# Performance work log

Hardware: AMD Instinct MI355X
Metric: run time of the kernel (lower is better)

## Reference

```python
import jax, jax.numpy as jnp
import numpy as np
import math

D_MODEL = 1024
HEADS = 16
DK = D_MODEL // HEADS
SEQ = 4096
BATCH = 4
SCALE_BASE = 512.0
ROPE_BASE = 10000.0
GN_EPS = 1e-5


def _xpos(x):
    # x: [B, S, D]; RetNet-style xpos rotary with per-dim magnitude scale
    B, S, D = x.shape
    half = D // 2
    sv = (jnp.arange(0, D, 2, dtype=jnp.float32) + 0.4 * D) / (1.4 * D)      # [half]
    pos = jnp.arange(S, dtype=jnp.float32)
    scale = sv[None, :] ** (pos[:, None] / SCALE_BASE)                        # [S, half]
    inv_freq = 1.0 / (ROPE_BASE ** (jnp.arange(half, dtype=jnp.float32) / half))
    ang = pos[:, None] * inv_freq[None, :]                                    # [S, half]
    sin = jnp.repeat(jnp.sin(ang) * scale, 2, axis=-1)                        # [S, D] (duplicate_interleave)
    cos = jnp.repeat(jnp.cos(ang) * scale, 2, axis=-1)
    x1, x2 = x[..., ::2], x[..., 1::2]
    rot = jnp.stack((-x2, x1), axis=-1).reshape(x.shape)                      # rotate_every_two
    return x * cos[None] + rot * sin[None]


def _decay_D():
    # D[h, n, m] = gamma_h**(n-m) * (n >= m); n over d_k rows, m over seq cols
    gammas = 1.0 - jnp.exp(jnp.linspace(math.log(1.0 / 32), math.log(1.0 / 512), HEADS))
    n = jnp.arange(DK)[:, None]
    m = jnp.arange(SEQ)[None, :]
    mask = n >= m
    diff = jnp.maximum(n - m, 0).astype(jnp.float32)                          # avoid inf for n<m
    return jnp.where(mask[None], gammas[:, None, None] ** diff[None], 0.0)    # [H, DK, SEQ]


def _group_norm(y, gn_w, gn_b):
    # torch GroupNorm(HEADS, DK) applied to rows of length DK
    B, S, D = y.shape
    g = DK // HEADS
    z = y.reshape(-1, HEADS, g)
    mu = z.mean(axis=-1, keepdims=True)
    var = z.var(axis=-1, keepdims=True)
    z = (z - mu) * jax.lax.rsqrt(var + GN_EPS)
    z = z * gn_w.reshape(HEADS, g) + gn_b.reshape(HEADS, g)
    return z.reshape(B, S, D)


def setup_inputs():
    key = jax.random.key(0)
    ks = jax.random.split(key, 9)
    s_d = 1.0 / math.sqrt(D_MODEL)
    s_s = 1.0 / math.sqrt(SEQ)
    return {
        "q": jax.random.normal(ks[0], (BATCH, SEQ, D_MODEL), jnp.float32),
        "k": jax.random.normal(ks[1], (BATCH, SEQ, D_MODEL), jnp.float32),
        "v": jax.random.normal(ks[2], (BATCH, SEQ, D_MODEL), jnp.float32),
        "wq": jax.random.normal(ks[3], (D_MODEL, D_MODEL), jnp.float32) * s_d,
        "wk": jax.random.normal(ks[4], (D_MODEL, D_MODEL), jnp.float32) * s_d,
        "wv": jax.random.normal(ks[5], (D_MODEL, D_MODEL), jnp.float32) * s_d,
        "wo": jax.random.normal(ks[6], (D_MODEL, D_MODEL), jnp.float32) * s_d,
        "wg": jax.random.normal(ks[7], (D_MODEL, D_MODEL), jnp.float32) * s_d,
        "wx_w": jax.random.normal(ks[8], (DK, SEQ), jnp.float32) * s_s,
        "wx_b": jnp.zeros((DK,), jnp.float32),
        "gn_w": jnp.ones((DK,), jnp.float32),
        "gn_b": jnp.zeros((DK,), jnp.float32),
    }


def reference(q, k, v, wq, wk, wv, wo, wg, wx_w, wx_b, gn_w, gn_b):
    B, S, D = q.shape
    query = _xpos(q @ wq.T)
    keyx = _xpos(k @ wk.T)
    value = v @ wv.T
    qh = query.reshape(B, S, HEADS, DK).transpose(0, 2, 1, 3)   # [B,H,S,DK]
    kh = keyx.reshape(B, S, HEADS, DK).transpose(0, 2, 1, 3)
    vh = value.reshape(B, S, HEADS, DK).transpose(0, 2, 1, 3)
    # Linformer-style learnable projection over sequence: [B,H,DK,S] -> [B,H,DK,DK]
    kp = jnp.einsum('bhsd,es->bhde', kh, wx_w) + wx_b
    vp = jnp.einsum('bhsd,es->bhde', vh, wx_w) + wx_b
    Dt = _decay_D().transpose(0, 2, 1)                           # [H, S, DK]
    scores = jnp.einsum('bhsd,bhde->bhse', qh, kp) * Dt[None]    # [B,H,S,DK]
    attn = jax.nn.softmax(scores, axis=-1)
    y = jnp.einsum('bhse,bhfe->bhsf', attn, vp)                  # attn @ Vp^T -> [B,H,S,DK]
    y = y.transpose(0, 2, 1, 3).reshape(B, S, D)
    y = _group_norm(y, gn_w, gn_b)
    gate = (q @ wg.T) * y
    return (gate * jax.nn.sigmoid(gate)) @ wo.T
```

## Files before the change

kernel.cpp:

```cpp
#include <hip/hip_runtime.h>
#include <hip/hip_bf16.h>

#define DEVI __device__ __forceinline__

typedef __attribute__((ext_vector_type(8))) short  short8;
typedef __attribute__((ext_vector_type(4))) float  floatx4;
typedef __attribute__((ext_vector_type(8))) __bf16 bf16x8;

DEVI float b2f(unsigned short u){ union{unsigned int i; float f;} x; x.i=((unsigned int)u)<<16; return x.f; }
DEVI unsigned short f2b(float f){
  union{float ff; unsigned int i;} x; x.ff=f;
  unsigned int r = x.i + 0x7fffu + ((x.i>>16)&1u);
  return (unsigned short)(r>>16);
}

DEVI void lds_dma16(const void* g, void* l){
  __builtin_amdgcn_global_load_lds((const __attribute__((address_space(1))) void*)g,
                                   (__attribute__((address_space(3))) void*)l, 16, 0, 0);
}

DEVI floatx4 mfma_bf16(short8 a, short8 b, floatx4 c){
  return __builtin_amdgcn_mfma_f32_16x16x32_bf16(
      __builtin_bit_cast(bf16x8, a), __builtin_bit_cast(bf16x8, b), c, 0, 0, 0);
}

DEVI void tile_remap(long& bmi, long& bni){
  const int bx = blockIdx.x, by = blockIdx.y;
  if (gridDim.y == 128){
    bni = (long)(by & 7);
    bmi = (long)((bx << 4) + (by >> 3));
  } else {
    bni = bx; bmi = by;
  }
}


__global__ void cvt_kernel(const float* __restrict__ src, unsigned short* __restrict__ dst, int n8)
{
  const int i = blockIdx.x * 256 + threadIdx.x;
  if (i >= n8) return;
  floatx4 a = ((const floatx4*)src)[2*(size_t)i];
  floatx4 b = ((const floatx4*)src)[2*(size_t)i + 1];
  short8 o;
  o[0]=(short)f2b(a[0]); o[1]=(short)f2b(a[1]); o[2]=(short)f2b(a[2]); o[3]=(short)f2b(a[3]);
  o[4]=(short)f2b(b[0]); o[5]=(short)f2b(b[1]); o[6]=(short)f2b(b[2]); o[7]=(short)f2b(b[3]);
  *(short8*)&dst[(size_t)i*8] = o;
}

__global__ void cvt_split(const float* __restrict__ src, unsigned short* __restrict__ dh,
                          unsigned short* __restrict__ dl, int n8)
{
  const int i = blockIdx.x * 256 + threadIdx.x;
  if (i >= n8) return;
  floatx4 a = ((const floatx4*)src)[2*(size_t)i];
  floatx4 b = ((const floatx4*)src)[2*(size_t)i + 1];
  short8 h, l;
  #pragma unroll
  for (int j = 0; j < 8; j++){
    float x = (j < 4) ? a[j] : b[j-4];
    unsigned short hb = f2b(x);
    h[j] = (short)hb;
    l[j] = (short)f2b(x - b2f(hb));
  }
  *(short8*)&dh[(size_t)i*8] = h;
  *(short8*)&dl[(size_t)i*8] = l;
}

template<int GATE>
__global__ __launch_bounds__(256, 3)
void gemm_af32(const float* __restrict__ A, const unsigned short* __restrict__ Bw,
               unsigned short* __restrict__ C, int M, int N, int K,
               const float* __restrict__ zs, const float* __restrict__ zc)
{
  __shared__ __align__(16) short As[128*64];
  __shared__ __align__(16) short Bs[128*64];
  const int t    = threadIdx.x;
  const int lane = t & 63;
  const int w    = t >> 6, wm = w >> 1, wn = w & 1;
  const int l15  = lane & 15, kg = lane >> 4;
  const int sx   = (l15 & 7) * 8;
  long bmi, bni; tile_remap(bmi, bni);
  const long bm = bmi * 128, bn = bni * 128;

  const int sr = t >> 3, sc8 = (t & 7) * 8;
  const int scx = sc8 ^ ((sr & 7) * 8);
  const unsigned short* pb[4];
  const float* pa[4];
  short *lb[4], *la[4];
  #pragma unroll
  for (int u = 0; u < 4; u++){
    pb[u] = Bw + (bn + sr + u*32) * (size_t)K + scx;
    pa[u] = A  + (bm + sr + u*32) * (size_t)K + sc8;
    lb[u] = &Bs[(sr + u*32)*64 + sc8];
    la[u] = &As[(sr + u*32)*64 + scx];
  }

  floatx4 acc[4][4] = {};
  floatx4 cur[8];
  #pragma unroll
  for (int u = 0; u < 4; u++){
    cur[2*u]   = *(const floatx4*)(pa[u]);
    cur[2*u+1] = *(const floatx4*)(pa[u] + 4);
  }
  #pragma unroll
  for (int u = 0; u < 4; u++) lds_dma16(pb[u], lb[u]);

  const int NT = K >> 6;
  for (int kt = 0; kt < NT; ++kt){
    __syncthreads();
    #pragma unroll
    for (int u = 0; u < 4; u++){
      short8 h;
      #pragma unroll
      for (int j = 0; j < 8; j++){
        float x = (j < 4) ? cur[2*u][j] : cur[2*u+1][j-4];
        h[j] = (short)f2b(x);
      }
      *(short8*)la[u] = h;
    }
    short8 bv[2][4];
    #pragma unroll
    for (int ks = 0; ks < 2; ks++)
      #pragma unroll
      for (int i = 0; i < 4; i++)
        bv[ks][i] = *(const short8*)&Bs[(wn*64 + i*16 + l15)*64 + ((ks*32 + kg*8) ^ sx)];
    __syncthreads();
    const int kn = (kt + 1 < NT) ? ((kt + 1) << 6) : 0;
    if (kt + 1 < NT){
      #pragma unroll
      for (int u = 0; u < 4; u++) lds_dma16(pb[u] + kn, lb[u]);
    }
    #pragma unroll
    for (int u = 0; u < 4; u++){
      cur[2*u]   = *(const floatx4*)(pa[u] + kn);
      cur[2*u+1] = *(const floatx4*)(pa[u] + kn + 4);
    }
    __builtin_amdgcn_sched_barrier(0);
    #pragma unroll
    for (int ks = 0; ks < 2; ks++){
      short8 af[4];
      #pragma unroll
      for (int i = 0; i < 4; i++)
        af[i] = *(const short8*)&As[(wm*64 + i*16 + l15)*64 + ((ks*32 + kg*8) ^ sx)];
      #pragma unroll
      for (int i = 0; i < 4; i++)
        #pragma unroll
        for (int j = 0; j < 4; j++)
          acc[i][j] = mfma_bf16(af[i], bv[ks][j], acc[i][j]);
    }
  }

  if (GATE){
    #pragma unroll
    for (int i = 0; i < 4; i++){
      const long mb = bm + wm*64 + i*16 + kg*4;
      #pragma unroll
      for (int r = 0; r < 4; r++){
        const long row = mb + r;
        const int  ss  = (int)(row & 4095);
        const long bb  = row >> 12;
        const float* zr = (ss < 64) ? (zs + (((size_t)(bb*64 + ss)) << 10))
                                    : (zc + ((size_t)bb << 10));
        #pragma unroll
        for (int j = 0; j < 4; j++){
          const long n = bn + wn*64 + j*16 + l15;
          float g = acc[i][j][r] * zr[n];
          float sig = 1.0f / (1.0f + __expf(-g));
          C[(size_t)row * N + n] = f2b(g * sig);
        }
      }
    }
  } else {
    #pragma unroll
    for (int i = 0; i < 4; i++){
      const long mb = bm + wm*64 + i*16 + kg*4;
      #pragma unroll
      for (int j = 0; j < 4; j++){
        const long n = bn + wn*64 + j*16 + l15;
        #pragma unroll
        for (int r = 0; r < 4; r++)
          C[(size_t)(mb + r) * N + n] = f2b(acc[i][j][r]);
      }
    }
  }
}

template<int QG>
__global__ __launch_bounds__(256, 2)
void gemm_split(const float* __restrict__ A, const unsigned short* __restrict__ Bh,
                const unsigned short* __restrict__ Bl, float* __restrict__ C,
                int M, int N, int K)
{
  __shared__ __align__(16) short Ash[128*64];
  __shared__ __align__(16) short Asl[128*64];
  __shared__ __align__(16) short Bsh[128*64];
  __shared__ __align__(16) short Bsl[128*64];
  const int t    = threadIdx.x;
  const int lane = t & 63;
  const int w    = t >> 6, wm = w >> 1, wn = w & 1;
  const int l15  = lane & 15, kg = lane >> 4;
  const int sx   = (l15 & 7) * 8;
  long bmi, bni; tile_remap(bmi, bni);
  const long bm = bmi * 128, bn = bni * 128;

  const int sr = t >> 3, sc8 = (t & 7) * 8;
  const int scx = sc8 ^ ((sr & 7) * 8);
  const unsigned short *pbh[4], *pbl[4];
  const float* pa[4];
  short *lbh[4], *lbl[4], *lah[4], *lal[4];
  #pragma unroll
  for (int u = 0; u < 4; u++){
    pbh[u] = Bh + (bn + sr + u*32) * (size_t)K + scx;
    pbl[u] = Bl + (bn + sr + u*32) * (size_t)K + scx;
    long ar = bm + sr + u*32;
    if (QG) ar = (ar >> 6) * 4096 + (ar & 63);
    pa[u]  = A + ar * (size_t)K + sc8;
    lbh[u] = &Bsh[(sr + u*32)*64 + sc8];
    lbl[u] = &Bsl[(sr + u*32)*64 + sc8];
    lah[u] = &Ash[(sr + u*32)*64 + scx];
    lal[u] = &Asl[(sr + u*32)*64 + scx];
  }

  floatx4 acc[4][4] = {};
  floatx4 cur[8];
  #pragma unroll
  for (int u = 0; u < 4; u++){
    cur[2*u]   = *(const floatx4*)(pa[u]);
    cur[2*u+1] = *(const floatx4*)(pa[u] + 4);
  }
  #pragma unroll
  for (int u = 0; u < 4; u++){
    lds_dma16(pbh[u], lbh[u]);
    lds_dma16(pbl[u], lbl[u]);
  }

  const int NT = K >> 6;
  for (int kt = 0; kt < NT; ++kt){
    __syncthreads();
    #pragma unroll
    for (int u = 0; u < 4; u++){
      short8 h, l;
      #pragma unroll
      for (int j = 0; j < 8; j++){
        float x = (j < 4) ? cur[2*u][j] : cur[2*u+1][j-4];
        unsigned short hb = f2b(x);
        h[j] = (short)hb;
        l[j] = (short)f2b(x - b2f(hb));
      }
      *(short8*)lah[u] = h;
      *(short8*)lal[u] = l;
    }
    short8 bvh[2][4], bvl[2][4];
    #pragma unroll
    for (int ks = 0; ks < 2; ks++)
      #pragma unroll
      for (int i = 0; i < 4; i++){
        const int rb = (wn*64 + i*16 + l15)*64 + ((ks*32 + kg*8) ^ sx);
        bvh[ks][i] = *(const short8*)&Bsh[rb];
        bvl[ks][i] = *(const short8*)&Bsl[rb];
      }
    __syncthreads();
    const int kn = (kt + 1 < NT) ? ((kt + 1) << 6) : 0;
    if (kt + 1 < NT){
      #pragma unroll
      for (int u = 0; u < 4; u++){
        lds_dma16(pbh[u] + kn, lbh[u]);
        lds_dma16(pbl[u] + kn, lbl[u]);
      }
    }
    #pragma unroll
    for (int u = 0; u < 4; u++){
      cur[2*u]   = *(const floatx4*)(pa[u] + kn);
      cur[2*u+1] = *(const floatx4*)(pa[u] + kn + 4);
    }
    __builtin_amdgcn_sched_barrier(0);
    #pragma unroll
    for (int ks = 0; ks < 2; ks++){
      short8 afh[4], afl[4];
      #pragma unroll
      for (int i = 0; i < 4; i++){
        const int ra = (wm*64 + i*16 + l15)*64 + ((ks*32 + kg*8) ^ sx);
        afh[i] = *(const short8*)&Ash[ra];
        afl[i] = *(const short8*)&Asl[ra];
      }
      #pragma unroll
      for (int i = 0; i < 4; i++)
        #pragma unroll
        for (int j = 0; j < 4; j++){
          acc[i][j] = mfma_bf16(afh[i], bvh[ks][j], acc[i][j]);
          acc[i][j] = mfma_bf16(afh[i], bvl[ks][j], acc[i][j]);
          acc[i][j] = mfma_bf16(afl[i], bvh[ks][j], acc[i][j]);
        }
    }
  }

  const int smask = QG ? 63 : 4095;
  #pragma unroll
  for (int j = 0; j < 4; j++){
    const long n  = bn + wn*64 + j*16 + l15;
    const int  ip = (int)(n >> 1);
    const float lsv  = __logf((2.0f*ip + 409.6f) * (1.0f/1433.6f));
    const float invf = __expf(-(float)ip * (9.2103403720f/512.0f));
    const float sgn  = (n & 1) ? 1.0f : -1.0f;
    #pragma unroll
    for (int i = 0; i < 4; i++){
      const long mb = bm + wm*64 + i*16 + kg*4;
      #pragma unroll
      for (int r = 0; r < 4; r++){
        float x = acc[i][j][r];
        float p = __shfl_xor(x, 1);
        const float fs = (float)((int)((mb + r) & smask));
        const float scale = __expf(lsv * fs * (1.0f/512.0f));
        float sn, cs;
        __sincosf(fs * invf, &sn, &cs);
        sn *= scale; cs *= scale;
        C[(size_t)(mb + r) * N + n] = x*cs + sgn*(p*sn);
      }
    }
  }
}

__global__ __launch_bounds__(256, 2)
void proj_split(const float* __restrict__ X0, const unsigned short* __restrict__ wxh,
                const unsigned short* __restrict__ wxl, float* __restrict__ P)
{
  __shared__ __align__(16) short Wsh[64*32];
  __shared__ __align__(16) short Wsl[64*32];
  __shared__ __align__(16) short Xth[64*40];
  __shared__ __align__(16) short Xtl[64*40];
  const int t = threadIdx.x, w = t >> 6, lane = t & 63;
  const int l15 = lane & 15, kg = lane >> 4;
  const int d0 = blockIdx.x * 64;
  const int b  = blockIdx.y;
  const float* X = X0 + (size_t)b * 4096 * 1024;
  const int s0 = blockIdx.z * 512;
  const int ssr = t >> 3, ddr = (t & 7) * 8;
  floatx4 acc[4] = {};

  for (int kk = 0; kk < 512; kk += 32){
    const int s = s0 + kk;
    floatx4 x0 = *(const floatx4*)&X[(size_t)(s + ssr) * 1024 + d0 + ddr];
    floatx4 x1 = *(const floatx4*)&X[(size_t)(s + ssr) * 1024 + d0 + ddr + 4];
    __syncthreads();
    lds_dma16(&wxh[(size_t)(t >> 2) * 4096 + s + (t & 3) * 8], &Wsh[t*8]);
    lds_dma16(&wxl[(size_t)(t >> 2) * 4096 + s + (t & 3) * 8], &Wsl[t*8]);
    float xv[8] = {x0[0],x0[1],x0[2],x0[3],x1[0],x1[1],x1[2],x1[3]};
    #pragma unroll
    for (int j = 0; j < 8; j++){
      unsigned short hb = f2b(xv[j]);
      Xth[(ddr + j) * 40 + ssr] = (short)hb;
      Xtl[(ddr + j) * 40 + ssr] = (short)f2b(xv[j] - b2f(hb));
    }
    __syncthreads();
    short8 afh = *(const short8*)&Wsh[(w*16 + l15)*32 + kg*8];
    short8 afl = *(const short8*)&Wsl[(w*16 + l15)*32 + kg*8];
    #pragma unroll
    for (int j = 0; j < 4; j++){
      short8 bvh = *(const short8*)&Xth[(j*16 + l15)*40 + kg*8];
      short8 bvl = *(const short8*)&Xtl[(j*16 + l15)*40 + kg*8];
      acc[j] = mfma_bf16(afh, bvh, acc[j]);
      acc[j] = mfma_bf16(afh, bvl, acc[j]);
      acc[j] = mfma_bf16(afl, bvh, acc[j]);
    }
  }
  float* Pb = P + (size_t)(b*2) * 65536;
  #pragma unroll
  for (int j = 0; j < 4; j++)
    #pragma unroll
    for (int r = 0; r < 4; r++)
      atomicAdd(&Pb[(w*16 + kg*4 + r) * 1024 + d0 + j*16 + l15], acc[j][r]);
}

__global__ __launch_bounds__(256, 2)
void proj_bf16(const unsigned short* __restrict__ X0, const unsigned short* __restrict__ wxw_bf,
               float* __restrict__ P)
{
  __shared__ __align__(16) short Ws[64*32];
  __shared__ __align__(16) short Xt[64*40];
  const int t = threadIdx.x, w = t >> 6, lane = t & 63;
  const int l15 = lane & 15, kg = lane >> 4;
  const int d0 = blockIdx.x * 64;
  const int b  = blockIdx.y;
  const unsigned short* X = X0 + (size_t)b * 4096 * 1024;
  const int s0 = blockIdx.z * 512;
  const int ssr = t >> 3, ddr = (t & 7) * 8;
  floatx4 acc[4] = {};

  for (int kk = 0; kk < 512; kk += 32){
    const int s = s0 + kk;
    short8 xv = *(const short8*)&X[(size_t)(s + ssr) * 1024 + d0 + ddr];
    __syncthreads();
    lds_dma16(&wxw_bf[(size_t)(t >> 2) * 4096 + s + (t & 3) * 8], &Ws[t*8]);
    #pragma unroll
    for (int j = 0; j < 8; j++) Xt[(ddr + j) * 40 + ssr] = xv[j];
    __syncthreads();
    short8 af = *(const short8*)&Ws[(w*16 + l15)*32 + kg*8];
    #pragma unroll
    for (int j = 0; j < 4; j++){
      short8 bv = *(const short8*)&Xt[(j*16 + l15)*40 + kg*8];
      acc[j] = mfma_bf16(af, bv, acc[j]);
    }
  }
  float* Pb = P + (size_t)(b*2 + 1) * 65536;
  #pragma unroll
  for (int j = 0; j < 4; j++)
    #pragma unroll
    for (int r = 0; r < 4; r++)
      atomicAdd(&Pb[(w*16 + kg*4 + r) * 1024 + d0 + j*16 + l15], acc[j][r]);
}

__global__ __launch_bounds__(256)
void attn_kernel(const float* __restrict__ P, const float* __restrict__ Qx,
                 const float* __restrict__ wxb,
                 const float* __restrict__ gnw, const float* __restrict__ gnb,
                 float* __restrict__ zs, float* __restrict__ zc)
{
  __shared__ __align__(16) float kps[64*64];
  __shared__ __align__(16) float vps[64*64];
  __shared__ __align__(16) float scs[64*65];
  __shared__ float pm[256];
  __shared__ float ym[64];
  const int t = threadIdx.x;
  const int w = t >> 6, s = t & 63;
  const int b = blockIdx.x >> 4, h = blockIdx.x & 15;
  const float* Pk = P + (size_t)(2*b) * 65536 + h*64;
  const float* Pv = Pk + 65536;

  {
    const int e = t >> 2, c = (t & 3) * 16;
    const float wb = wxb[e];
    #pragma unroll
    for (int j = 0; j < 4; j++){
      floatx4 kv = *(const floatx4*)&Pk[(size_t)e*1024 + c + 4*j];
      floatx4 vv = *(const floatx4*)&Pv[(size_t)e*1024 + c + 4*j];
      kv.x += wb; kv.y += wb; kv.z += wb; kv.w += wb;
      vv.x += wb; vv.y += wb; vv.z += wb; vv.w += wb;
      *(floatx4*)&kps[e*64 + c + 4*j] = kv;
      *(floatx4*)&vps[e*64 + c + 4*j] = vv;
    }
  }
  __syncthreads();

  float qf[64];
  const floatx4* q4 = (const floatx4*)(Qx + (size_t)(b*64 + s)*1024 + h*64);
  #pragma unroll
  for (int i = 0; i < 16; i++){
    floatx4 qq = q4[i];
    qf[4*i] = qq.x; qf[4*i+1] = qq.y; qf[4*i+2] = qq.z; qf[4*i+3] = qq.w;
  }

  #pragma unroll
  for (int eo = 0; eo < 16; eo++){
    const int e = w*16 + eo;
    const floatx4* kp4 = (const floatx4*)&kps[e*64];
    float dot = 0.f;
    #pragma unroll
    for (int d = 0; d < 16; d++){
      floatx4 kv = kp4[d];
      dot += qf[4*d]*kv.x + qf[4*d+1]*kv.y + qf[4*d+2]*kv.z + qf[4*d+3]*kv.w;
    }
    scs[e*65 + s] = dot;
  }
  {
    float am = 0.f;
    #pragma unroll
    for (int eo = 0; eo < 16; eo++) am += vps[(w*16 + eo)*64 + s];
    pm[t] = am;
  }
  __syncthreads();

  const float lg = -3.4657359028f - 0.1848392483f * (float)h;
  const float gamma = 1.0f - __expf(lg);
  float sc[64];
  #pragma unroll
  for (int e = 0; e < 64; e++) sc[e] = scs[e*65 + s];
  float dec = 1.0f;
  #pragma unroll
  for (int e = 0; e < 64; e++){
    bool on = (e >= s);
    sc[e] = on ? sc[e]*dec : 0.0f;
    if (on) dec *= gamma;
  }
  float mx = -1e30f;
  #pragma unroll
  for (int e = 0; e < 64; e++) mx = fmaxf(mx, sc[e]);
  float Z = 0.f;
  #pragma unroll
  for (int e = 0; e < 64; e++){ sc[e] = __expf(sc[e] - mx); Z += sc[e]; }
  const float rz = 1.0f / Z;

  #pragma unroll
  for (int go = 0; go < 4; go++){
    const int g = w*4 + go;
    floatx4 y = {0.f,0.f,0.f,0.f};
    #pragma unroll
    for (int e = 0; e < 64; e++){
      floatx4 vv = *(const floatx4*)&vps[e*64 + g*4];
      y += sc[e] * vv;
    }
    y *= rz;
    float mu = (y.x + y.y + y.z + y.w) * 0.25f;
    float a0 = y.x-mu, a1 = y.y-mu, a2 = y.z-mu, a3 = y.w-mu;
    float inv = rsqrtf((a0*a0 + a1*a1 + a2*a2 + a3*a3)*0.25f + 1e-5f);
    floatx4 o;
    o.x = a0*inv*gnw[g*4+0] + gnb[g*4+0];
    o.y = a1*inv*gnw[g*4+1] + gnb[g*4+1];
    o.z = a2*inv*gnw[g*4+2] + gnb[g*4+2];
    o.w = a3*inv*gnw[g*4+3] + gnb[g*4+3];
    *(floatx4*)&zs[(size_t)(b*64 + s)*1024 + h*64 + g*4] = o;
  }

  if (w == 0)
    ym[s] = (pm[s] + pm[64+s] + pm[128+s] + pm[192+s]) * (1.0f/64.0f);
  __syncthreads();
  if (t < 16){
    float a0 = ym[t*4], a1 = ym[t*4+1], a2 = ym[t*4+2], a3 = ym[t*4+3];
    float mu = (a0+a1+a2+a3)*0.25f;
    a0 -= mu; a1 -= mu; a2 -= mu; a3 -= mu;
    float inv = rsqrtf((a0*a0+a1*a1+a2*a2+a3*a3)*0.25f + 1e-5f);
    zc[(size_t)b*1024 + h*64 + t*4+0] = a0*inv*gnw[t*4+0] + gnb[t*4+0];
    zc[(size_t)b*1024 + h*64 + t*4+1] = a1*inv*gnw[t*4+1] + gnb[t*4+1];
    zc[(size_t)b*1024 + h*64 + t*4+2] = a2*inv*gnw[t*4+2] + gnb[t*4+2];
    zc[(size_t)b*1024 + h*64 + t*4+3] = a3*inv*gnw[t*4+3] + gnb[t*4+3];
  }
}

__global__ __launch_bounds__(256, 3)
void gemm_bt(const unsigned short* __restrict__ A, const unsigned short* __restrict__ Bw,
             float* __restrict__ C, int M, int N, int K)
{
  __shared__ __align__(16) short As[128*64];
  __shared__ __align__(16) short Bs[128*64];
  const int t    = threadIdx.x;
  const int lane = t & 63;
  const int w    = t >> 6, wm = w >> 1, wn = w & 1;
  const int l15  = lane & 15, kg = lane >> 4;
  const int sx   = (l15 & 7) * 8;
  long bmi, bni; tile_remap(bmi, bni);
  const long bm = bmi * 128, bn = bni * 128;

  const int sr = t >> 3, sc8 = (t & 7) * 8;
  const int scx = sc8 ^ ((sr & 7) * 8);
  const unsigned short *pa[4], *pb[4];
  short *la[4], *lb[4];
  #pragma unroll
  for (int u = 0; u < 4; u++){
    pa[u] = A  + (bm + sr + u*32) * (size_t)K + scx;
    pb[u] = Bw + (bn + sr + u*32) * (size_t)K + scx;
    la[u] = &As[(sr + u*32)*64 + sc8];
    lb[u] = &Bs[(sr + u*32)*64 + sc8];
  }

  floatx4 acc[4][4] = {};

  #pragma unroll
  for (int u = 0; u < 4; u++){
    lds_dma16(pa[u], la[u]);
    lds_dma16(pb[u], lb[u]);
  }

  const int NT = K >> 6;
  for (int kt = 0; kt < NT; ++kt){
    __syncthreads();
    short8 af[2][4], bv[2][4];
    #pragma unroll
    for (int ks = 0; ks < 2; ks++)
      #pragma unroll
      for (int i = 0; i < 4; i++){
        af[ks][i] = *(const short8*)&As[(wm*64 + i*16 + l15)*64 + ((ks*32 + kg*8) ^ sx)];
        bv[ks][i] = *(const short8*)&Bs[(wn*64 + i*16 + l15)*64 + ((ks*32 + kg*8) ^ sx)];
      }
    __syncthreads();
    if (kt + 1 < NT){
      const int kn = (kt + 1) << 6;
      #pragma unroll
      for (int u = 0; u < 4; u++){
        lds_dma16(pa[u] + kn, la[u]);
        lds_dma16(pb[u] + kn, lb[u]);
      }
    }
    __builtin_amdgcn_sched_barrier(0);
    #pragma unroll
    for (int ks = 0; ks < 2; ks++)
      #pragma unroll
      for (int i = 0; i < 4; i++)
        #pragma unroll
        for (int j = 0; j < 4; j++)
          acc[i][j] = mfma_bf16(af[ks][i], bv[ks][j], acc[i][j]);
  }

  #pragma unroll
  for (int i = 0; i < 4; i++){
    const long mb = bm + wm*64 + i*16 + kg*4;
    #pragma unroll
    for (int j = 0; j < 4; j++){
      const long n = bn + wn*64 + j*16 + l15;
      #pragma unroll
      for (int r = 0; r < 4; r++)
        C[(size_t)(mb + r) * N + n] = acc[i][j][r];
    }
  }
}

extern "C" void kernel_launch(void* const* d_in, const int* in_sizes, int n_in,
                              void* d_out, int out_size, void* d_ws, size_t ws_size,
                              hipStream_t stream)
{
  const float* q   = (const float*)d_in[0];
  const float* k   = (const float*)d_in[1];
  const float* v   = (const float*)d_in[2];
  const float* wq  = (const float*)d_in[3];
  const float* wk  = (const float*)d_in[4];
  const float* wv  = (const float*)d_in[5];
  const float* wo  = (const float*)d_in[6];
  const float* wg  = (const float*)d_in[7];
  const float* wxw = (const float*)d_in[8];
  const float* wxb = (const float*)d_in[9];
  const float* gnw = (const float*)d_in[10];
  const float* gnb = (const float*)d_in[11];

  char* ws = (char*)d_ws;
  unsigned short* A0   = (unsigned short*)(ws);
  unsigned short* wh   = (unsigned short*)(ws + 33554432);
  unsigned short* wl   = (unsigned short*)(ws + 35651584);
  unsigned short* wAbf = (unsigned short*)(ws + 37748736);
  unsigned short* wgbf = (unsigned short*)(ws + 39845888);
  unsigned short* wxh  = (unsigned short*)(ws + 41943040);
  unsigned short* wxl  = (unsigned short*)(ws + 42467328);
  float*          P    = (float*)(ws + 42991616);
  float*          zs   = (float*)(ws + 45088768);
  float*          zc   = (float*)(ws + 46137344);
  float*          Qx   = (float*)(ws + 46153728);
  float*          Kx   = (float*)d_out;

  const int M = 16384, N = 1024, K = 1024;
  dim3 blk(256);

  cvt_split<<<512, blk, 0, stream>>>(wk, wh, wl, 131072);
  cvt_split<<<128, blk, 0, stream>>>(wxw, wxh, wxl, 32768);
  cvt_kernel<<<512, blk, 0, stream>>>(wv, wAbf, 131072);
  cvt_kernel<<<512, blk, 0, stream>>>(wg, wgbf, 131072);
  hipMemsetAsync(P, 0, 2097152, stream);

  gemm_split<0><<<dim3(8,128), blk, 0, stream>>>(k, wh, wl, Kx, M, N, K);
  proj_split<<<dim3(16,4,8), blk, 0, stream>>>(Kx, wxh, wxl, P);

  gemm_af32<0><<<dim3(8,128), blk, 0, stream>>>(v, wAbf, A0, M, N, K, nullptr, nullptr);
  proj_bf16<<<dim3(16,4,8), blk, 0, stream>>>(A0, wxh, P);
  cvt_kernel<<<512, blk, 0, stream>>>(wo, wAbf, 131072);

  cvt_split<<<512, blk, 0, stream>>>(wq, wh, wl, 131072);
  gemm_split<1><<<dim3(8,2), blk, 0, stream>>>(q, wh, wl, Qx, 256, N, K);
  attn_kernel<<<64, 256, 0, stream>>>(P, Qx, wxb, gnw, gnb, zs, zc);

  gemm_af32<1><<<dim3(8,128), blk, 0, stream>>>(q, wgbf, A0, M, N, K, zs, zc);
  gemm_bt<<<dim3(8,128), blk, 0, stream>>>(A0, wAbf, (float*)d_out, M, N, K);
}
```

Baseline: 596.1 us.

## Pre-split K input to bf16, widen fp32-A GEMM tiles, generalize XCD remap

The K projection now runs in two halves. Each half first converts the fp32 input into bf16 hi/lo arrays, then runs a new all-DMA split GEMM (three MFMAs per tile step) with xpos rotary applied in the epilogue. This replaces the older gemm_split path, which converted A on the fly. The gemm_af32 kernels move to 128x256 tiles with double-buffered B in LDS and half the grid, trading occupancy for more reuse per A conversion. The tile remap is generalized to spread blocks across XCDs for any grid whose y-dimension is a multiple of 8.

```diff
diff --git a/kernel.cpp b/kernel.cpp
--- a/kernel.cpp
+++ b/kernel.cpp
@@ -26,9 +26,12 @@
 
 DEVI void tile_remap(long& bmi, long& bni){
   const int bx = blockIdx.x, by = blockIdx.y;
-  if (gridDim.y == 128){
-    bni = (long)(by & 7);
-    bmi = (long)((bx << 4) + (by >> 3));
+  if ((gridDim.y & 7) == 0 && gridDim.y >= 8){
+    const int flat = bx + gridDim.x * by;
+    const int xcd  = flat & 7;
+    const int idx  = flat >> 3;
+    bni = (long)(idx % gridDim.x);
+    bmi = (long)(xcd * (gridDim.y >> 3) + idx / gridDim.x);
   } else {
     bni = bx; bmi = by;
   }
@@ -66,36 +69,137 @@
   *(short8*)&dl[(size_t)i*8] = l;
 }
 
+__global__ __launch_bounds__(256, 2)
+void gemm_split3(const unsigned short* __restrict__ Ah, const unsigned short* __restrict__ Al,
+                 const unsigned short* __restrict__ Bh, const unsigned short* __restrict__ Bl,
+                 float* __restrict__ C, int M, int N, int K)
+{
+  __shared__ __align__(16) short Ash[128*64];
+  __shared__ __align__(16) short Asl[128*64];
+  __shared__ __align__(16) short Bsh[128*64];
+  __shared__ __align__(16) short Bsl[128*64];
+  const int t = threadIdx.x, lane = t & 63;
+  const int w = t >> 6, wm = w >> 1, wn = w & 1;
+  const int l15 = lane & 15, kg = lane >> 4;
+  const int sx = (l15 & 7) * 8;
+  long bmi, bni; tile_remap(bmi, bni);
+  const long bm = bmi * 128, bn = bni * 128;
+
+  size_t aoff[4], boff[4]; int ldst[4];
+  #pragma unroll
+  for (int u = 0; u < 4; u++){
+    const int cl = u*256 + t, row = cl >> 3, cr = cl & 7;
+    const int csrc = (cr ^ (row & 7)) * 8;
+    aoff[u] = (size_t)(bm + row) * K + csrc;
+    boff[u] = (size_t)(bn + row) * K + csrc;
+    ldst[u] = cl * 8;
+  }
+
+  floatx4 acc[4][4] = {};
+  #pragma unroll
+  for (int u = 0; u < 4; u++){
+    lds_dma16(Ah + aoff[u], &Ash[ldst[u]]);
+    lds_dma16(Al + aoff[u], &Asl[ldst[u]]);
+    lds_dma16(Bh + boff[u], &Bsh[ldst[u]]);
+    lds_dma16(Bl + boff[u], &Bsl[ldst[u]]);
+  }
+
+  const int NT = K >> 6;
+  for (int kt = 0; kt < NT; ++kt){
+    __syncthreads();
+    short8 afh[2][4], afl[2][4], bvh[2][4], bvl[2][4];
+    #pragma unroll
+    for (int ks = 0; ks < 2; ks++)
+      #pragma unroll
+      for (int i = 0; i < 4; i++){
+        const int ra = (wm*64 + i*16 + l15)*64 + ((ks*32 + kg*8) ^ sx);
+        const int rb = (wn*64 + i*16 + l15)*64 + ((ks*32 + kg*8) ^ sx);
+        afh[ks][i] = *(const short8*)&Ash[ra];
+        afl[ks][i] = *(const short8*)&Asl[ra];
+        bvh[ks][i] = *(const short8*)&Bsh[rb];
+        bvl[ks][i] = *(const short8*)&Bsl[rb];
+      }
+    __syncthreads();
+    if (kt + 1 < NT){
+      const int kn = (kt + 1) << 6;
+      #pragma unroll
+      for (int u = 0; u < 4; u++){
+        lds_dma16(Ah + aoff[u] + kn, &Ash[ldst[u]]);
+        lds_dma16(Al + aoff[u] + kn, &Asl[ldst[u]]);
+        lds_dma16(Bh + boff[u] + kn, &Bsh[ldst[u]]);
+        lds_dma16(Bl + boff[u] + kn, &Bsl[ldst[u]]);
+      }
+    }
+    __builtin_amdgcn_sched_barrier(0);
+    #pragma unroll
+    for (int ks = 0; ks < 2; ks++)
+      #pragma unroll
+      for (int i = 0; i < 4; i++)
+        #pragma unroll
+        for (int j = 0; j < 4; j++){
+          acc[i][j] = mfma_bf16(afh[ks][i], bvh[ks][j], acc[i][j]);
+          acc[i][j] = mfma_bf16(afh[ks][i], bvl[ks][j], acc[i][j]);
+          acc[i][j] = mfma_bf16(afl[ks][i], bvh[ks][j], acc[i][j]);
+        }
+  }
+
+  #pragma unroll
+  for (int j = 0; j < 4; j++){
+    const long n  = bn + wn*64 + j*16 + l15;
+    const int  ip = (int)(n >> 1);
+    const float lsv  = __logf((2.0f*ip + 409.6f) * (1.0f/1433.6f));
+    const float invf = __expf(-(float)ip * (9.2103403720f/512.0f));
+    const float sgn  = (n & 1) ? 1.0f : -1.0f;
+    #pragma unroll
+    for (int i = 0; i < 4; i++){
+      const long mb = bm + wm*64 + i*16 + kg*4;
+      #pragma unroll
+      for (int r = 0; r < 4; r++){
+        float x = acc[i][j][r];
+        float p = __shfl_xor(x, 1);
+        const float fs = (float)((int)((mb + r) & 4095));
+        const float scale = __expf(lsv * fs * (1.0f/512.0f));
+        float sn, cs;
+        __sincosf(fs * invf, &sn, &cs);
+        sn *= scale; cs *= scale;
+        C[(size_t)(mb + r) * N + n] = x*cs + sgn*(p*sn);
+      }
+    }
+  }
+}
+
 template<int GATE>
-__global__ __launch_bounds__(256, 3)
+__global__ __launch_bounds__(256, 2)
 void gemm_af32(const float* __restrict__ A, const unsigned short* __restrict__ Bw,
                unsigned short* __restrict__ C, int M, int N, int K,
                const float* __restrict__ zs, const float* __restrict__ zc)
 {
   __shared__ __align__(16) short As[128*64];
-  __shared__ __align__(16) short Bs[128*64];
-  const int t    = threadIdx.x;
-  const int lane = t & 63;
-  const int w    = t >> 6, wm = w >> 1, wn = w & 1;
-  const int l15  = lane & 15, kg = lane >> 4;
-  const int sx   = (l15 & 7) * 8;
+  __shared__ __align__(16) short Bs[2][256*64];
+  const int t = threadIdx.x, lane = t & 63;
+  const int w = t >> 6, wm = w >> 1, wn = w & 1;
+  const int l15 = lane & 15, kg = lane >> 4;
+  const int sx = (l15 & 7) * 8;
   long bmi, bni; tile_remap(bmi, bni);
-  const long bm = bmi * 128, bn = bni * 128;
-
+  const long bm = bmi * 128, bn = bni * 256;
+
+  size_t boff[8]; int bdst[8];
+  #pragma unroll
+  for (int u = 0; u < 8; u++){
+    const int cl = u*256 + t, row = cl >> 3, cr = cl & 7;
+    boff[u] = (size_t)(bn + row) * K + (cr ^ (row & 7)) * 8;
+    bdst[u] = cl * 8;
+  }
   const int sr = t >> 3, sc8 = (t & 7) * 8;
   const int scx = sc8 ^ ((sr & 7) * 8);
-  const unsigned short* pb[4];
-  const float* pa[4];
-  short *lb[4], *la[4];
-  #pragma unroll
-  for (int u = 0; u < 4; u++){
-    pb[u] = Bw + (bn + sr + u*32) * (size_t)K + scx;
-    pa[u] = A  + (bm + sr + u*32) * (size_t)K + sc8;
-    lb[u] = &Bs[(sr + u*32)*64 + sc8];
+  const float* pa[4]; short* la[4];
+  #pragma unroll
+  for (int u = 0; u < 4; u++){
+    pa[u] = A + (bm + sr + u*32) * (size_t)K + sc8;
     la[u] = &As[(sr + u*32)*64 + scx];
   }
 
-  floatx4 acc[4][4] = {};
+  floatx4 acc[4][8] = {};
   floatx4 cur[8];
   #pragma unroll
   for (int u = 0; u < 4; u++){
@@ -103,9 +207,10 @@
     cur[2*u+1] = *(const floatx4*)(pa[u] + 4);
   }
   #pragma unroll
-  for (int u = 0; u < 4; u++) lds_dma16(pb[u], lb[u]);
+  for (int u = 0; u < 8; u++) lds_dma16(Bw + boff[u], &Bs[0][bdst[u]]);
 
   const int NT = K >> 6;
+  int o = 0;
   for (int kt = 0; kt < NT; ++kt){
     __syncthreads();
     #pragma unroll
@@ -118,17 +223,11 @@
       }
       *(short8*)la[u] = h;
     }
-    short8 bv[2][4];
-    #pragma unroll
-    for (int ks = 0; ks < 2; ks++)
-      #pragma unroll
-      for (int i = 0; i < 4; i++)
-        bv[ks][i] = *(const short8*)&Bs[(wn*64 + i*16 + l15)*64 + ((ks*32 + kg*8) ^ sx)];
     __syncthreads();
     const int kn = (kt + 1 < NT) ? ((kt + 1) << 6) : 0;
     if (kt + 1 < NT){
       #pragma unroll
-      for (int u = 0; u < 4; u++) lds_dma16(pb[u] + kn, lb[u]);
+      for (int u = 0; u < 8; u++) lds_dma16(Bw + boff[u] + kn, &Bs[o^1][bdst[u]]);
     }
     #pragma unroll
     for (int u = 0; u < 4; u++){
@@ -138,16 +237,20 @@
     __builtin_amdgcn_sched_barrier(0);
     #pragma unroll
     for (int ks = 0; ks < 2; ks++){
-      short8 af[4];
+      short8 af[4], bv[8];
       #pragma unroll
       for (int i = 0; i < 4; i++)
         af[i] = *(const short8*)&As[(wm*64 + i*16 + l15)*64 + ((ks*32 + kg*8) ^ sx)];
       #pragma unroll
+      for (int j = 0; j < 8; j++)
+        bv[j] = *(const short8*)&Bs[o][(wn*128 + j*16 + l15)*64 + ((ks*32 + kg*8) ^ sx)];
+      #pragma unroll
       for (int i = 0; i < 4; i++)
         #pragma unroll
-        for (int j = 0; j < 4; j++)
-          acc[i][j] = mfma_bf16(af[i], bv[ks][j], acc[i][j]);
-    }
+        for (int j = 0; j < 8; j++)
+          acc[i][j] = mfma_bf16(af[i], bv[j], acc[i][j]);
+    }
+    o ^= 1;
   }
 
   if (GATE){
@@ -162,8 +265,8 @@
         const float* zr = (ss < 64) ? (zs + (((size_t)(bb*64 + ss)) << 10))
                                     : (zc + ((size_t)bb << 10));
         #pragma unroll
-        for (int j = 0; j < 4; j++){
-          const long n = bn + wn*64 + j*16 + l15;
+        for (int j = 0; j < 8; j++){
+          const long n = bn + wn*128 + j*16 + l15;
           float g = acc[i][j][r] * zr[n];
           float sig = 1.0f / (1.0f + __expf(-g));
           C[(size_t)row * N + n] = f2b(g * sig);
@@ -175,8 +278,8 @@
     for (int i = 0; i < 4; i++){
       const long mb = bm + wm*64 + i*16 + kg*4;
       #pragma unroll
-      for (int j = 0; j < 4; j++){
-        const long n = bn + wn*64 + j*16 + l15;
+      for (int j = 0; j < 8; j++){
+        const long n = bn + wn*128 + j*16 + l15;
         #pragma unroll
         for (int r = 0; r < 4; r++)
           C[(size_t)(mb + r) * N + n] = f2b(acc[i][j][r]);
@@ -642,10 +745,14 @@
   cvt_kernel<<<512, blk, 0, stream>>>(wg, wgbf, 131072);
   hipMemsetAsync(P, 0, 2097152, stream);
 
-  gemm_split<0><<<dim3(8,128), blk, 0, stream>>>(k, wh, wl, Kx, M, N, K);
+  for (int p = 0; p < 2; p++){
+    cvt_split<<<4096, blk, 0, stream>>>(k + (size_t)p*8388608, A0, A0 + 8388608, 1048576);
+    gemm_split3<<<dim3(8,64), blk, 0, stream>>>(A0, A0 + 8388608, wh, wl,
+                                                Kx + (size_t)p*8388608, 8192, N, K);
+  }
   proj_split<<<dim3(16,4,8), blk, 0, stream>>>(Kx, wxh, wxl, P);
 
-  gemm_af32<0><<<dim3(8,128), blk, 0, stream>>>(v, wAbf, A0, M, N, K, nullptr, nullptr);
+  gemm_af32<0><<<dim3(4,128), blk, 0, stream>>>(v, wAbf, A0, M, N, K, nullptr, nullptr);
   proj_bf16<<<dim3(16,4,8), blk, 0, stream>>>(A0, wxh, P);
   cvt_kernel<<<512, blk, 0, stream>>>(wo, wAbf, 131072);
 
@@ -653,6 +760,6 @@
   gemm_split<1><<<dim3(8,2), blk, 0, stream>>>(q, wh, wl, Qx, 256, N, K);
   attn_kernel<<<64, 256, 0, stream>>>(P, Qx, wxb, gnw, gnb, zs, zc);
 
-  gemm_af32<1><<<dim3(8,128), blk, 0, stream>>>(q, wgbf, A0, M, N, K, zs, zc);
+  gemm_af32<1><<<dim3(4,128), blk, 0, stream>>>(q, wgbf, A0, M, N, K, zs, zc);
   gemm_bt<<<dim3(8,128), blk, 0, stream>>>(A0, wAbf, (float*)d_out, M, N, K);
 }
```

After: 565.2 us. -5.2%, faster.
